# Optimization experiments

Measured on AMD Instinct MI355X. Metric: run time of the kernel, lower is better.

## Reference

```python
import jax, jax.numpy as jnp
import numpy as np

S, H, P, NL, PL = 128, 1024, 1024, 2, 32  # string_size, hidden, program_size, layers, program_length
T_IN, T_OUT = 64, 64


def _run_lstm(xs, h0, c0, layers):
    """Multi-layer LSTM over sequence xs [T, in]. PyTorch gate order i,f,g,o.
    h0, c0: [NL, H]. Returns (top-layer outputs [T, H], hT [NL,H], cT [NL,H])."""
    hs, cs = [], []
    for l, (Wih, Whh, bih, bhh) in enumerate(layers):
        b = bih + bhh
        def step(carry, x, Wih=Wih, Whh=Whh, b=b):
            h, c = carry
            g = Wih @ x + Whh @ h + b           # [4H]
            i, f, gg, o = jnp.split(g, 4)
            c = jax.nn.sigmoid(f) * c + jax.nn.sigmoid(i) * jnp.tanh(gg)
            h = jax.nn.sigmoid(o) * jnp.tanh(c)
            return (h, c), h
        (hT, cT), xs = jax.lax.scan(step, (h0[l], c0[l]), xs)
        hs.append(hT); cs.append(cT)
    return xs, jnp.stack(hs), jnp.stack(cs)


def setup_inputs() -> dict:
    key = jax.random.key(0)
    keys = iter(jax.random.split(key, 64))
    bound = 1.0 / np.sqrt(H)
    def u(shape):
        return jax.random.uniform(next(keys), shape, minval=-bound, maxval=bound, dtype=jnp.float32)
    d = {}
    for pre, in0 in (("in", S), ("out", S), ("pr", H)):
        for l in range(NL):
            isz = in0 if l == 0 else H
            d[f"{pre}_Wih{l}"] = u((4 * H, isz))
            d[f"{pre}_Whh{l}"] = u((4 * H, H))
            d[f"{pre}_bih{l}"] = u((4 * H,))
            d[f"{pre}_bhh{l}"] = u((4 * H,))
    d["lin_W"] = u((P, H))
    d["lin_b"] = u((P,))
    d["input_seq"] = jax.random.randint(next(keys), (T_IN,), 0, S)
    d["output_seq"] = jax.random.randint(next(keys), (T_OUT,), 0, S)
    return d


def reference(in_Wih0, in_Whh0, in_bih0, in_bhh0, in_Wih1, in_Whh1, in_bih1, in_bhh1,
              out_Wih0, out_Whh0, out_bih0, out_bhh0, out_Wih1, out_Whh1, out_bih1, out_bhh1,
              pr_Wih0, pr_Whh0, pr_bih0, pr_bhh0, pr_Wih1, pr_Whh1, pr_bih1, pr_bhh1,
              lin_W, lin_b, input_seq, output_seq):
    in_layers = [(in_Wih0, in_Whh0, in_bih0, in_bhh0), (in_Wih1, in_Whh1, in_bih1, in_bhh1)]
    out_layers = [(out_Wih0, out_Whh0, out_bih0, out_bhh0), (out_Wih1, out_Whh1, out_bih1, out_bhh1)]
    pr_layers = [(pr_Wih0, pr_Whh0, pr_bih0, pr_bhh0), (pr_Wih1, pr_Whh1, pr_bih1, pr_bhh1)]

    x_in = jax.nn.one_hot(input_seq, S, dtype=jnp.float32)    # [T_IN, S]
    x_out = jax.nn.one_hot(output_seq, S, dtype=jnp.float32)  # [T_OUT, S]

    h = jnp.zeros((NL, H), dtype=jnp.float32)
    c = jnp.zeros((NL, H), dtype=jnp.float32)
    _, h, c = _run_lstm(x_in, h, c, in_layers)
    _, h, c = _run_lstm(x_out, h, c, out_layers)

    # Faithful to source: previous_hidden is set once and never updated inside the loop,
    # so the program LSTM sees the SAME input vector at every decode step.
    prev_h = h[-1]                                            # [H]
    xs = jnp.broadcast_to(prev_h, (PL, H))
    ys, h, c = _run_lstm(xs, h, c, pr_layers)                 # [PL, H]
    return ys @ lin_W.T + lin_b                                # [PL, P]
```

## Files before the change

kernel.cpp:

```cpp
#include <hip/hip_runtime.h>
#include <hip/hip_fp16.h>
#include <cmath>

#define HDIM 1024
#define TPB 512
#define NWG 256
#define M4 4194304ull
#define WS_WOFF 327680ull
#define CVT_TOTAL 42991616ull
#define WS_NEEDED (WS_WOFF + CVT_TOTAL * 2ull)

typedef unsigned long long ulong64;
typedef unsigned int uint32;
typedef _Float16 h2f __attribute__((ext_vector_type(2)));

__device__ __forceinline__ ulong64 ld_g8(const ulong64* p) {
  return __hip_atomic_load(p, __ATOMIC_RELAXED, __HIP_MEMORY_SCOPE_AGENT);
}
__device__ __forceinline__ void st_gu(uint32* p, uint32 v) {
  __hip_atomic_store(p, v, __ATOMIC_RELAXED, __HIP_MEMORY_SCOPE_AGENT);
}
__device__ __forceinline__ void st_gi(int* p, int v) {
  __hip_atomic_store(p, v, __ATOMIC_RELAXED, __HIP_MEMORY_SCOPE_AGENT);
}

__device__ __forceinline__ float sigm(float x) { return 1.f / (1.f + __expf(-x)); }
__device__ __forceinline__ float tanh_f(float x) {
  float e = __expf(2.f * x);
  return 1.f - 2.f / (e + 1.f);
}

__device__ __forceinline__ float f4dot(float4 wf, float4 xf, float acc) {
  union { float4 f; h2f h[4]; } w, x;
  w.f = wf; x.f = xf;
#pragma unroll
  for (int i = 0; i < 4; ++i) {
#if __has_builtin(__builtin_amdgcn_fdot2)
    acc = __builtin_amdgcn_fdot2(w.h[i], x.h[i], acc, false);
#else
    acc = fmaf((float)w.h[i].x, (float)x.h[i].x, acc);
    acc = fmaf((float)w.h[i].y, (float)x.h[i].y, acc);
#endif
  }
  return acc;
}

__global__ void __launch_bounds__(TPB, 2) rf16_kernel(
    const float* __restrict__ in_Wih0, const float* __restrict__ in_bih0, const float* __restrict__ in_bhh0,
    const float* __restrict__ in_bih1, const float* __restrict__ in_bhh1,
    const float* __restrict__ out_Wih0, const float* __restrict__ out_bih0, const float* __restrict__ out_bhh0,
    const float* __restrict__ out_bih1, const float* __restrict__ out_bhh1,
    const float* __restrict__ pr_bih0, const float* __restrict__ pr_bhh0,
    const float* __restrict__ pr_bih1, const float* __restrict__ pr_bhh1,
    const float* __restrict__ lin_b,
    const int* __restrict__ in_seq, const int* __restrict__ out_seq,
    float* __restrict__ out, float* __restrict__ ws)
{
  const int tid = threadIdx.x, wg = blockIdx.x;
  const int wv = tid >> 6, lane = tid & 63;
  const int grp = lane >> 4, gl = lane & 15;
  const int cell = (wg << 2) + (wv & 3);
  const bool isL1 = wv < 4;
  const int rowi = (grp << 10) + cell;
  const bool chkWG = (wg < 8);

  const __half* wb = (const __half*)((const char*)ws + WS_WOFF);
  uint32* h0M = (uint32*)((char*)ws + 4096);
  uint32* h1M = (uint32*)((char*)ws + 20480);
  int* FL = (int*)((char*)ws + 36864);
  int* myFlag = FL + ((wg & 7) << 8);

  __shared__ __align__(16) ulong64 xaP[2][128], xbP[2][128];

  float c_reg = 0.f, pre0v = 0.f;
  float bA, bB, bC, lbias = 0.f;
  if (isL1) {
    bA = in_bih1[rowi] + in_bhh1[rowi];
    bB = out_bih1[rowi] + out_bhh1[rowi];
    bC = pr_bih1[rowi] + pr_bhh1[rowi];
  } else {
    bA = in_bih0[rowi] + in_bhh0[rowi];
    bB = out_bih0[rowi] + out_bhh0[rowi];
    bC = pr_bih0[rowi] + pr_bhh0[rowi];
    lbias = lin_b[cell];
  }

  int fail = 0;
  float4 wreg[16];
  float4 lw0, lw1;

  auto preload8 = [&](const __half* wrow, int base) {
    const float4* w4 = (const float4*)wrow;
#pragma unroll
    for (int j = 0; j < 8; ++j) wreg[base + j] = w4[j * 16 + gl];
  };
  auto dotx = [&](int base, const ulong64* xp, float acc) {
    const __half* x = (const __half*)xp;
#pragma unroll
    for (int j = 0; j < 8; ++j)
      acc = f4dot(wreg[base + j], *(const float4*)(x + (j * 16 + gl) * 8), acc);
    return acc;
  };
  auto red16 = [&](float v) {
#pragma unroll
    for (int o = 1; o < 16; o <<= 1) v += __shfl_xor(v, o, 64);
    return v;
  };
  auto wred64 = [&](float v) {
#pragma unroll
    for (int o = 1; o < 64; o <<= 1) v += __shfl_xor(v, o, 64);
    return v;
  };
  auto tags_ok = [&](const ulong64* d, int tag) {
    bool ok = true;
#pragma unroll
    for (int i = 0; i < 8; ++i)
      ok &= (((int)((d[i] >> 16) & 0xFFFF)) == tag) & (((int)(d[i] >> 48)) == tag);
    return ok;
  };
  auto pack_lds = [&](const ulong64* d, ulong64* dst) {
    uint32 q[8];
#pragma unroll
    for (int i = 0; i < 8; ++i)
      q[i] = (uint32)(d[i] & 0xFFFF) | ((uint32)((d[i] >> 32) & 0xFFFF) << 16);
    dst[4 * lane]     = (ulong64)q[0] | ((ulong64)q[1] << 32);
    dst[4 * lane + 1] = (ulong64)q[2] | ((ulong64)q[3] << 32);
    dst[4 * lane + 2] = (ulong64)q[4] | ((ulong64)q[5] << 32);
    dst[4 * lane + 3] = (ulong64)q[6] | ((ulong64)q[7] << 32);
  };
  auto fetch_pack = [&](const uint32* T, int stream, int tag, ulong64* dst) {
    if (fail) return;
    const int slot = tag & 3;
    if (chkWG) {
      const ulong64* sl = (const ulong64*)(T + (slot << 10)) + (wg << 6) + lane;
      int spins = 0;
      for (;;) {
        ulong64 w = ld_g8(sl);
        bool ok = (((int)((w >> 16) & 0xFFFF)) == tag) & (((int)(w >> 48)) == tag);
        if (__all(ok)) break;
        if (++spins > (1 << 20)) { fail = 1; break; }
      }
      if (!fail && lane < 8)
        st_gi(FL + (lane << 8) + (stream << 7) + (slot << 4) + wg, tag);
    }
    {
      const ulong64* fp = (const ulong64*)(myFlag + (stream << 7) + (slot << 4));
      int spins = 0;
      for (;;) {
        ulong64 f0 = ld_g8(fp), f1 = ld_g8(fp + 1);
        ulong64 f2 = ld_g8(fp + 2), f3 = ld_g8(fp + 3);
        bool ok = (((int)f0) == tag) & (((int)(f0 >> 32)) == tag) &
                  (((int)f1) == tag) & (((int)(f1 >> 32)) == tag) &
                  (((int)f2) == tag) & (((int)(f2 >> 32)) == tag) &
                  (((int)f3) == tag) & (((int)(f3 >> 32)) == tag);
        if (ok) break;
        if (++spins > (1 << 20)) { fail = 1; return; }
        __builtin_amdgcn_s_sleep(1);
      }
    }
    const ulong64* src = (const ulong64*)(T + (slot << 10)) + (lane << 3);
    ulong64 d[8];
    int spins = 0;
    for (;;) {
#pragma unroll
      for (int i = 0; i < 8; ++i) d[i] = ld_g8(src + i);
      if (__all(tags_ok(d, tag))) break;
      if (++spins > (1 << 16)) { fail = 1; return; }
    }
    pack_lds(d, dst);
  };
  auto zero_pack = [&](ulong64* dst) {
#pragma unroll
    for (int i = 0; i < 4; ++i) dst[4 * lane + i] = 0ull;
  };
  auto produce = [&](float v, uint32* T, int tag) {
    float gi = __shfl(v, 0, 64), gf = __shfl(v, 16, 64);
    float gc = __shfl(v, 32, 64), go = __shfl(v, 48, 64);
    float c2 = sigm(gf) * c_reg + sigm(gi) * tanh_f(gc);
    c_reg = c2;
    if (lane == 0) {
      uint32 w = ((uint32)tag << 16) | (uint32)__half_as_ushort(__float2half(sigm(go) * tanh_f(c2)));
      st_gu(T + ((tag & 3) << 10) + cell, w);
    }
  };

  if (!isL1) {
    int idx = in_seq[0];
    float v = bA + in_Wih0[(size_t)rowi * 128 + idx];
    produce(v, h0M, 1);
  }

  if (isL1) {
    preload8(wb + 0 * M4 + (size_t)rowi * 1024, 0);
    preload8(wb + 1 * M4 + (size_t)rowi * 1024, 8);
  } else {
    preload8(wb + 2 * M4 + (size_t)rowi * 1024, 0);
  }

#pragma unroll 1
  for (int s = 2; s <= 128; ++s) {
    if (s == 65 && !isL1) preload8(wb + 5 * M4 + (size_t)rowi * 1024, 0);
    if (s == 66 && isL1) {
      preload8(wb + 3 * M4 + (size_t)rowi * 1024, 0);
      preload8(wb + 4 * M4 + (size_t)rowi * 1024, 8);
    }
    float wcol = 0.f;
    if (!isL1) {
      int idx = (s < 65) ? in_seq[s - 1] : out_seq[s - 65];
      wcol = ((s < 65) ? in_Wih0 : out_Wih0)[(size_t)rowi * 128 + idx];
    }
    if (wv == 0) fetch_pack(h0M, 0, s - 1, xaP[s & 1]);
    if (wv == 1) {
      if (s == 2) zero_pack(xbP[0]);
      else fetch_pack(h1M, 1, s - 1, xbP[s & 1]);
    }
    __syncthreads();
    if (isL1) {
      float v = dotx(0, xaP[s & 1], 0.f);
      v = dotx(8, xbP[s & 1], v);
      v = red16(v) + ((s < 66) ? bA : bB);
      produce(v, h1M, s);
    } else {
      float v = red16(dotx(0, xaP[s & 1], 0.f)) + ((s < 65) ? bA : bB) + wcol;
      produce(v, h0M, s);
    }
  }

  if (wv == 0) fetch_pack(h0M, 0, 128, xaP[1]);
  if (wv == 1) fetch_pack(h1M, 1, 128, xbP[1]);
  __syncthreads();
  if (isL1) {
    float v = dotx(0, xaP[1], 0.f);
    v = dotx(8, xbP[1], v);
    v = red16(v) + bB;
    produce(v, h1M, 129);
  }

  if (!isL1) {
    preload8(wb + 9 * M4 + (size_t)rowi * 1024, 0);
    preload8(wb + 8 * M4 + (size_t)rowi * 1024, 8);
  }
  if (wv == 0) fetch_pack(h0M, 0, 128, xaP[0]);
  if (wv == 1) fetch_pack(h1M, 1, 129, xbP[0]);
  __syncthreads();
  if (!isL1) {
    pre0v = red16(dotx(0, xbP[0], 0.f)) + bC;
    float v = red16(dotx(8, xaP[0], 0.f)) + pre0v;
    produce(v, h0M, 130);
  }

  if (isL1) {
    preload8(wb + 6 * M4 + (size_t)rowi * 1024, 0);
    preload8(wb + 7 * M4 + (size_t)rowi * 1024, 8);
  } else {
#pragma unroll
    for (int j = 0; j < 8; ++j) wreg[j] = wreg[8 + j];
    const float4* lwp = (const float4*)(wb + 10 * M4 + (size_t)cell * 1024);
    lw0 = lwp[lane * 2]; lw1 = lwp[lane * 2 + 1];
  }

#pragma unroll 1
  for (int s = 131; s <= 162; ++s) {
    const int tb = (s == 131) ? 129 : s - 1;
    if (wv == 0) fetch_pack(h0M, 0, s - 1, xaP[s & 1]);
    if (wv == 1) fetch_pack(h1M, 1, tb, xbP[s & 1]);
    __syncthreads();
    if (isL1) {
      float v = dotx(0, xaP[s & 1], 0.f);
      v = dotx(8, xbP[s & 1], v);
      v = red16(v) + bC;
      produce(v, h1M, s);
    } else {
      if (s >= 132) {
        const __half* x = (const __half*)xbP[s & 1];
        float a = f4dot(lw0, *(const float4*)(x + lane * 16), 0.f);
        a = f4dot(lw1, *(const float4*)(x + lane * 16 + 8), a);
        float r = wred64(a) + lbias;
        if (lane == 0) out[(size_t)(s - 132) * 1024 + cell] = r;
      }
      if (s <= 161) {
        float v = red16(dotx(0, xaP[s & 1], 0.f)) + pre0v;
        produce(v, h0M, s);
      }
    }
  }

  if (wv == 1) fetch_pack(h1M, 1, 162, xbP[1]);
  __syncthreads();
  if (!isL1) {
    const __half* x = (const __half*)xbP[1];
    float a = f4dot(lw0, *(const float4*)(x + lane * 16), 0.f);
    a = f4dot(lw1, *(const float4*)(x + lane * 16 + 8), a);
    float r = wred64(a) + lbias;
    if (lane == 0) out[(size_t)31 * 1024 + cell] = r;
  }
}

struct CvtArgs { const float* s[11]; };

__global__ void __launch_bounds__(256) cvt_kernel(CvtArgs a, __half* dst) {
  size_t i = ((size_t)blockIdx.x * 256 + threadIdx.x) * 8;
  if (i >= CVT_TOTAL) return;
  const float* sp;
  if (i < 10 * M4) sp = a.s[i >> 22] + (i & (M4 - 1));
  else sp = a.s[10] + (i - 10 * M4);
  float4 f0 = ((const float4*)sp)[0];
  float4 f1 = ((const float4*)sp)[1];
  __half2 o[4];
  o[0] = __float22half2_rn(make_float2(f0.x, f0.y));
  o[1] = __float22half2_rn(make_float2(f0.z, f0.w));
  o[2] = __float22half2_rn(make_float2(f1.x, f1.y));
  o[3] = __float22half2_rn(make_float2(f1.z, f1.w));
  *((float4*)(dst + i)) = *(float4*)o;
}

extern "C" void kernel_launch(void* const* d_in, const int* in_sizes, int n_in,
                              void* d_out, int out_size, void* d_ws, size_t ws_size,
                              hipStream_t stream) {
  (void)in_sizes; (void)n_in; (void)out_size;
  if (ws_size < WS_NEEDED) return;
  (void)hipMemsetAsync(d_ws, 0, 45056, stream);
  const float* F[26];
  for (int i = 0; i < 26; ++i) F[i] = (const float*)d_in[i];
  const int* iseq = (const int*)d_in[26];
  const int* oseq = (const int*)d_in[27];

  CvtArgs ca;
  ca.s[0] = F[4];  ca.s[1] = F[5];  ca.s[2] = F[1];
  ca.s[3] = F[12]; ca.s[4] = F[13]; ca.s[5] = F[9];
  ca.s[6] = F[20]; ca.s[7] = F[21]; ca.s[8] = F[17];
  ca.s[9] = F[16]; ca.s[10] = F[24];
  __half* wdst = (__half*)((char*)d_ws + WS_WOFF);
  cvt_kernel<<<dim3((unsigned)(CVT_TOTAL / 8 / 256)), dim3(256), 0, stream>>>(ca, wdst);
  rf16_kernel<<<dim3(NWG), dim3(TPB), 0, stream>>>(
      F[0], F[2], F[3], F[6], F[7],
      F[8], F[10], F[11], F[14], F[15],
      F[18], F[19], F[22], F[23],
      F[25], iseq, oseq, (float*)d_out, (float*)d_ws);
}
```

Measured before the change: 654.6 us.

## Replace flag-based step barrier with replicated mirrored hidden-state buffers

Checker workgroups no longer publish per-slot flags that every workgroup polls before reading the shared hidden-state table. Instead they copy the validated tagged words into eight mirror copies, and each workgroup spins directly on its own mirror using the embedded tags. This removes one polling round-trip per timestep and spreads reads across replicas. The cost is eight times more store traffic per checker, a larger memset, and doubled LDS array declarations.

New measurement: 671.3 us. 2.5% more time.

```diff
diff --git a/kernel.cpp b/kernel.cpp
--- a/kernel.cpp
+++ b/kernel.cpp
@@ -17,10 +17,10 @@
 __device__ __forceinline__ ulong64 ld_g8(const ulong64* p) {
   return __hip_atomic_load(p, __ATOMIC_RELAXED, __HIP_MEMORY_SCOPE_AGENT);
 }
+__device__ __forceinline__ void st_g8(ulong64* p, ulong64 v) {
+  __hip_atomic_store(p, v, __ATOMIC_RELAXED, __HIP_MEMORY_SCOPE_AGENT);
+}
 __device__ __forceinline__ void st_gu(uint32* p, uint32 v) {
-  __hip_atomic_store(p, v, __ATOMIC_RELAXED, __HIP_MEMORY_SCOPE_AGENT);
-}
-__device__ __forceinline__ void st_gi(int* p, int v) {
   __hip_atomic_store(p, v, __ATOMIC_RELAXED, __HIP_MEMORY_SCOPE_AGENT);
 }
 
@@ -67,10 +67,11 @@
   const __half* wb = (const __half*)((const char*)ws + WS_WOFF);
   uint32* h0M = (uint32*)((char*)ws + 4096);
   uint32* h1M = (uint32*)((char*)ws + 20480);
-  int* FL = (int*)((char*)ws + 36864);
-  int* myFlag = FL + ((wg & 7) << 8);
-
-  __shared__ __align__(16) ulong64 xaP[2][128], xbP[2][128];
+  ulong64* h0Mir = (ulong64*)((char*)ws + 36864);
+  ulong64* h1Mir = (ulong64*)((char*)ws + 36864 + 131072);
+  const int myMir = (wg & 7) << 11;
+
+  __shared__ __align__(16) ulong64 xaP[2][256], xbP[2][256];
 
   float c_reg = 0.f, pre0v = 0.f;
   float bA, bB, bC, lbias = 0.f;
@@ -128,44 +129,35 @@
     dst[4 * lane + 2] = (ulong64)q[4] | ((ulong64)q[5] << 32);
     dst[4 * lane + 3] = (ulong64)q[6] | ((ulong64)q[7] << 32);
   };
-  auto fetch_pack = [&](const uint32* T, int stream, int tag, ulong64* dst) {
+  auto fetch_pack = [&](const uint32* T, ulong64* Mir, int tag, ulong64* dst) {
     if (fail) return;
     const int slot = tag & 3;
     if (chkWG) {
       const ulong64* sl = (const ulong64*)(T + (slot << 10)) + (wg << 6) + lane;
+      ulong64 w = 0;
       int spins = 0;
       for (;;) {
-        ulong64 w = ld_g8(sl);
+        w = ld_g8(sl);
         bool ok = (((int)((w >> 16) & 0xFFFF)) == tag) & (((int)(w >> 48)) == tag);
         if (__all(ok)) break;
         if (++spins > (1 << 20)) { fail = 1; break; }
       }
-      if (!fail && lane < 8)
-        st_gi(FL + (lane << 8) + (stream << 7) + (slot << 4) + wg, tag);
-    }
-    {
-      const ulong64* fp = (const ulong64*)(myFlag + (stream << 7) + (slot << 4));
-      int spins = 0;
-      for (;;) {
-        ulong64 f0 = ld_g8(fp), f1 = ld_g8(fp + 1);
-        ulong64 f2 = ld_g8(fp + 2), f3 = ld_g8(fp + 3);
-        bool ok = (((int)f0) == tag) & (((int)(f0 >> 32)) == tag) &
-                  (((int)f1) == tag) & (((int)(f1 >> 32)) == tag) &
-                  (((int)f2) == tag) & (((int)(f2 >> 32)) == tag) &
-                  (((int)f3) == tag) & (((int)(f3 >> 32)) == tag);
-        if (ok) break;
-        if (++spins > (1 << 20)) { fail = 1; return; }
-        __builtin_amdgcn_s_sleep(1);
+      if (!fail) {
+        const int widx = (slot << 9) + (wg << 6) + lane;
+#pragma unroll
+        for (int m = 0; m < 8; ++m)
+          st_g8(Mir + (m << 11) + widx, w);
       }
     }
-    const ulong64* src = (const ulong64*)(T + (slot << 10)) + (lane << 3);
+    const ulong64* src = Mir + myMir + (slot << 9) + (lane << 3);
     ulong64 d[8];
     int spins = 0;
     for (;;) {
 #pragma unroll
       for (int i = 0; i < 8; ++i) d[i] = ld_g8(src + i);
       if (__all(tags_ok(d, tag))) break;
-      if (++spins > (1 << 16)) { fail = 1; return; }
+      if (++spins > (1 << 20)) { fail = 1; return; }
+      __builtin_amdgcn_s_sleep(1);
     }
     pack_lds(d, dst);
   };
@@ -209,10 +201,10 @@
       int idx = (s < 65) ? in_seq[s - 1] : out_seq[s - 65];
       wcol = ((s < 65) ? in_Wih0 : out_Wih0)[(size_t)rowi * 128 + idx];
     }
-    if (wv == 0) fetch_pack(h0M, 0, s - 1, xaP[s & 1]);
+    if (wv == 0) fetch_pack(h0M, h0Mir, s - 1, xaP[s & 1]);
     if (wv == 1) {
       if (s == 2) zero_pack(xbP[0]);
-      else fetch_pack(h1M, 1, s - 1, xbP[s & 1]);
+      else fetch_pack(h1M, h1Mir, s - 1, xbP[s & 1]);
     }
     __syncthreads();
     if (isL1) {
@@ -226,8 +218,8 @@
     }
   }
 
-  if (wv == 0) fetch_pack(h0M, 0, 128, xaP[1]);
-  if (wv == 1) fetch_pack(h1M, 1, 128, xbP[1]);
+  if (wv == 0) fetch_pack(h0M, h0Mir, 128, xaP[1]);
+  if (wv == 1) fetch_pack(h1M, h1Mir, 128, xbP[1]);
   __syncthreads();
   if (isL1) {
     float v = dotx(0, xaP[1], 0.f);
@@ -240,8 +232,8 @@
     preload8(wb + 9 * M4 + (size_t)rowi * 1024, 0);
     preload8(wb + 8 * M4 + (size_t)rowi * 1024, 8);
   }
-  if (wv == 0) fetch_pack(h0M, 0, 128, xaP[0]);
-  if (wv == 1) fetch_pack(h1M, 1, 129, xbP[0]);
+  if (wv == 0) fetch_pack(h0M, h0Mir, 128, xaP[0]);
+  if (wv == 1) fetch_pack(h1M, h1Mir, 129, xbP[0]);
   __syncthreads();
   if (!isL1) {
     pre0v = red16(dotx(0, xbP[0], 0.f)) + bC;
@@ -262,8 +254,8 @@
 #pragma unroll 1
   for (int s = 131; s <= 162; ++s) {
     const int tb = (s == 131) ? 129 : s - 1;
-    if (wv == 0) fetch_pack(h0M, 0, s - 1, xaP[s & 1]);
-    if (wv == 1) fetch_pack(h1M, 1, tb, xbP[s & 1]);
+    if (wv == 0) fetch_pack(h0M, h0Mir, s - 1, xaP[s & 1]);
+    if (wv == 1) fetch_pack(h1M, h1Mir, tb, xbP[s & 1]);
     __syncthreads();
     if (isL1) {
       float v = dotx(0, xaP[s & 1], 0.f);
@@ -285,7 +277,7 @@
     }
   }
 
-  if (wv == 1) fetch_pack(h1M, 1, 162, xbP[1]);
+  if (wv == 1) fetch_pack(h1M, h1Mir, 162, xbP[1]);
   __syncthreads();
   if (!isL1) {
     const __half* x = (const __half*)xbP[1];
@@ -319,7 +311,7 @@
                               hipStream_t stream) {
   (void)in_sizes; (void)n_in; (void)out_size;
   if (ws_size < WS_NEEDED) return;
-  (void)hipMemsetAsync(d_ws, 0, 45056, stream);
+  (void)hipMemsetAsync(d_ws, 0, 299008, stream);
   const float* F[26];
   for (int i = 0; i < 26; ++i) F[i] = (const float*)d_in[i];
   const int* iseq = (const int*)d_in[26];
```

## Fuse fp32-to-fp16 weight conversion into the persistent LSTM kernel's register preloads

Applied to the files above, without the earlier changes.

Removes the separate conversion kernel that turned about 43M fp32 weights into fp16 in workspace. Each thread now reads its fp32 weight rows directly and converts them to half in registers during preload, for both the LSTM matrices and the final linear layer. This drops one full read-and-write pass over the weights and one kernel launch, and shrinks the workspace to the small flag/state area. In exchange, each preload inside the recurrence reads twice as many bytes, so the stalls at the sequence boundaries get longer. The shared-memory pack buffers are also doubled in size, and kernel arguments are now passed as a struct.

Measured after the change: 693.2 us. 5.9% more time.

```diff
diff --git a/kernel.cpp b/kernel.cpp
--- a/kernel.cpp
+++ b/kernel.cpp
@@ -5,10 +5,7 @@
 #define HDIM 1024
 #define TPB 512
 #define NWG 256
-#define M4 4194304ull
-#define WS_WOFF 327680ull
-#define CVT_TOTAL 42991616ull
-#define WS_NEEDED (WS_WOFF + CVT_TOTAL * 2ull)
+#define WS_NEEDED 45056ull
 
 typedef unsigned long long ulong64;
 typedef unsigned int uint32;
@@ -45,16 +42,22 @@
   return acc;
 }
 
-__global__ void __launch_bounds__(TPB, 2) rf16_kernel(
-    const float* __restrict__ in_Wih0, const float* __restrict__ in_bih0, const float* __restrict__ in_bhh0,
-    const float* __restrict__ in_bih1, const float* __restrict__ in_bhh1,
-    const float* __restrict__ out_Wih0, const float* __restrict__ out_bih0, const float* __restrict__ out_bhh0,
-    const float* __restrict__ out_bih1, const float* __restrict__ out_bhh1,
-    const float* __restrict__ pr_bih0, const float* __restrict__ pr_bhh0,
-    const float* __restrict__ pr_bih1, const float* __restrict__ pr_bhh1,
-    const float* __restrict__ lin_b,
-    const int* __restrict__ in_seq, const int* __restrict__ out_seq,
-    float* __restrict__ out, float* __restrict__ ws)
+__device__ __forceinline__ float4 cvt8(float4 a, float4 b) {
+  float4 r;
+  ((__half2*)&r)[0] = __float22half2_rn(make_float2(a.x, a.y));
+  ((__half2*)&r)[1] = __float22half2_rn(make_float2(a.z, a.w));
+  ((__half2*)&r)[2] = __float22half2_rn(make_float2(b.x, b.y));
+  ((__half2*)&r)[3] = __float22half2_rn(make_float2(b.z, b.w));
+  return r;
+}
+
+struct KArgs {
+  const float* W[26];
+  const int* iseq; const int* oseq;
+  float* out; float* ws;
+};
+
+__global__ void __launch_bounds__(TPB, 2) rf16_kernel(KArgs a)
 {
   const int tid = threadIdx.x, wg = blockIdx.x;
   const int wv = tid >> 6, lane = tid & 63;
@@ -64,35 +67,39 @@
   const int rowi = (grp << 10) + cell;
   const bool chkWG = (wg < 8);
 
-  const __half* wb = (const __half*)((const char*)ws + WS_WOFF);
+  float* ws = a.ws;
   uint32* h0M = (uint32*)((char*)ws + 4096);
   uint32* h1M = (uint32*)((char*)ws + 20480);
   int* FL = (int*)((char*)ws + 36864);
   int* myFlag = FL + ((wg & 7) << 8);
 
-  __shared__ __align__(16) ulong64 xaP[2][128], xbP[2][128];
+  __shared__ __align__(16) ulong64 xaP[2][256], xbP[2][256];
 
   float c_reg = 0.f, pre0v = 0.f;
   float bA, bB, bC, lbias = 0.f;
   if (isL1) {
-    bA = in_bih1[rowi] + in_bhh1[rowi];
-    bB = out_bih1[rowi] + out_bhh1[rowi];
-    bC = pr_bih1[rowi] + pr_bhh1[rowi];
+    bA = a.W[6][rowi] + a.W[7][rowi];
+    bB = a.W[14][rowi] + a.W[15][rowi];
+    bC = a.W[22][rowi] + a.W[23][rowi];
   } else {
-    bA = in_bih0[rowi] + in_bhh0[rowi];
-    bB = out_bih0[rowi] + out_bhh0[rowi];
-    bC = pr_bih0[rowi] + pr_bhh0[rowi];
-    lbias = lin_b[cell];
+    bA = a.W[2][rowi] + a.W[3][rowi];
+    bB = a.W[10][rowi] + a.W[11][rowi];
+    bC = a.W[18][rowi] + a.W[19][rowi];
+    lbias = a.W[25][cell];
   }
 
   int fail = 0;
   float4 wreg[16];
   float4 lw0, lw1;
 
-  auto preload8 = [&](const __half* wrow, int base) {
-    const float4* w4 = (const float4*)wrow;
-#pragma unroll
-    for (int j = 0; j < 8; ++j) wreg[base + j] = w4[j * 16 + gl];
+  auto preload8 = [&](const float* mat, int base) {
+    const float4* w4 = (const float4*)(mat + (size_t)rowi * 1024);
+#pragma unroll
+    for (int j = 0; j < 8; ++j) {
+      float4 p = w4[(j * 16 + gl) * 2];
+      float4 q = w4[(j * 16 + gl) * 2 + 1];
+      wreg[base + j] = cvt8(p, q);
+    }
   };
   auto dotx = [&](int base, const ulong64* xp, float acc) {
     const __half* x = (const __half*)xp;
@@ -185,29 +192,29 @@
   };
 
   if (!isL1) {
-    int idx = in_seq[0];
-    float v = bA + in_Wih0[(size_t)rowi * 128 + idx];
+    int idx = a.iseq[0];
+    float v = bA + a.W[0][(size_t)rowi * 128 + idx];
     produce(v, h0M, 1);
   }
 
   if (isL1) {
-    preload8(wb + 0 * M4 + (size_t)rowi * 1024, 0);
-    preload8(wb + 1 * M4 + (size_t)rowi * 1024, 8);
+    preload8(a.W[4], 0);
+    preload8(a.W[5], 8);
   } else {
-    preload8(wb + 2 * M4 + (size_t)rowi * 1024, 0);
+    preload8(a.W[1], 0);
   }
 
 #pragma unroll 1
   for (int s = 2; s <= 128; ++s) {
-    if (s == 65 && !isL1) preload8(wb + 5 * M4 + (size_t)rowi * 1024, 0);
+    if (s == 65 && !isL1) preload8(a.W[9], 0);
     if (s == 66 && isL1) {
-      preload8(wb + 3 * M4 + (size_t)rowi * 1024, 0);
-      preload8(wb + 4 * M4 + (size_t)rowi * 1024, 8);
+      preload8(a.W[12], 0);
+      preload8(a.W[13], 8);
     }
     float wcol = 0.f;
     if (!isL1) {
-      int idx = (s < 65) ? in_seq[s - 1] : out_seq[s - 65];
-      wcol = ((s < 65) ? in_Wih0 : out_Wih0)[(size_t)rowi * 128 + idx];
+      int idx = (s < 65) ? a.iseq[s - 1] : a.oseq[s - 65];
+      wcol = ((s < 65) ? a.W[0] : a.W[8])[(size_t)rowi * 128 + idx];
     }
     if (wv == 0) fetch_pack(h0M, 0, s - 1, xaP[s & 1]);
     if (wv == 1) {
@@ -237,8 +244,8 @@
   }
 
   if (!isL1) {
-    preload8(wb + 9 * M4 + (size_t)rowi * 1024, 0);
-    preload8(wb + 8 * M4 + (size_t)rowi * 1024, 8);
+    preload8(a.W[16], 0);
+    preload8(a.W[17], 8);
   }
   if (wv == 0) fetch_pack(h0M, 0, 128, xaP[0]);
   if (wv == 1) fetch_pack(h1M, 1, 129, xbP[0]);
@@ -250,13 +257,15 @@
   }
 
   if (isL1) {
-    preload8(wb + 6 * M4 + (size_t)rowi * 1024, 0);
-    preload8(wb + 7 * M4 + (size_t)rowi * 1024, 8);
+    preload8(a.W[20], 0);
+    preload8(a.W[21], 8);
   } else {
 #pragma unroll
     for (int j = 0; j < 8; ++j) wreg[j] = wreg[8 + j];
-    const float4* lwp = (const float4*)(wb + 10 * M4 + (size_t)cell * 1024);
-    lw0 = lwp[lane * 2]; lw1 = lwp[lane * 2 + 1];
+    const float4* lwp = (const float4*)(a.W[24] + (size_t)cell * 1024);
+    float4 a0 = lwp[lane * 4], a1 = lwp[lane * 4 + 1];
+    float4 a2 = lwp[lane * 4 + 2], a3 = lwp[lane * 4 + 3];
+    lw0 = cvt8(a0, a1); lw1 = cvt8(a2, a3);
   }
 
 #pragma unroll 1
@@ -273,10 +282,10 @@
     } else {
       if (s >= 132) {
         const __half* x = (const __half*)xbP[s & 1];
-        float a = f4dot(lw0, *(const float4*)(x + lane * 16), 0.f);
-        a = f4dot(lw1, *(const float4*)(x + lane * 16 + 8), a);
-        float r = wred64(a) + lbias;
-        if (lane == 0) out[(size_t)(s - 132) * 1024 + cell] = r;
+        float a0 = f4dot(lw0, *(const float4*)(x + lane * 16), 0.f);
+        a0 = f4dot(lw1, *(const float4*)(x + lane * 16 + 8), a0);
+        float r = wred64(a0) + lbias;
+        if (lane == 0) a.out[(size_t)(s - 132) * 1024 + cell] = r;
       }
       if (s <= 161) {
         float v = red16(dotx(0, xaP[s & 1], 0.f)) + pre0v;
@@ -289,29 +298,11 @@
   __syncthreads();
   if (!isL1) {
     const __half* x = (const __half*)xbP[1];
-    float a = f4dot(lw0, *(const float4*)(x + lane * 16), 0.f);
-    a = f4dot(lw1, *(const float4*)(x + lane * 16 + 8), a);
-    float r = wred64(a) + lbias;
-    if (lane == 0) out[(size_t)31 * 1024 + cell] = r;
-  }
-}
-
-struct CvtArgs { const float* s[11]; };
-
-__global__ void __launch_bounds__(256) cvt_kernel(CvtArgs a, __half* dst) {
-  size_t i = ((size_t)blockIdx.x * 256 + threadIdx.x) * 8;
-  if (i >= CVT_TOTAL) return;
-  const float* sp;
-  if (i < 10 * M4) sp = a.s[i >> 22] + (i & (M4 - 1));
-  else sp = a.s[10] + (i - 10 * M4);
-  float4 f0 = ((const float4*)sp)[0];
-  float4 f1 = ((const float4*)sp)[1];
-  __half2 o[4];
-  o[0] = __float22half2_rn(make_float2(f0.x, f0.y));
-  o[1] = __float22half2_rn(make_float2(f0.z, f0.w));
-  o[2] = __float22half2_rn(make_float2(f1.x, f1.y));
-  o[3] = __float22half2_rn(make_float2(f1.z, f1.w));
-  *((float4*)(dst + i)) = *(float4*)o;
+    float a0 = f4dot(lw0, *(const float4*)(x + lane * 16), 0.f);
+    a0 = f4dot(lw1, *(const float4*)(x + lane * 16 + 8), a0);
+    float r = wred64(a0) + lbias;
+    if (lane == 0) a.out[(size_t)31 * 1024 + cell] = r;
+  }
 }
 
 extern "C" void kernel_launch(void* const* d_in, const int* in_sizes, int n_in,
@@ -319,22 +310,12 @@
                               hipStream_t stream) {
   (void)in_sizes; (void)n_in; (void)out_size;
   if (ws_size < WS_NEEDED) return;
-  (void)hipMemsetAsync(d_ws, 0, 45056, stream);
-  const float* F[26];
-  for (int i = 0; i < 26; ++i) F[i] = (const float*)d_in[i];
-  const int* iseq = (const int*)d_in[26];
-  const int* oseq = (const int*)d_in[27];
-
-  CvtArgs ca;
-  ca.s[0] = F[4];  ca.s[1] = F[5];  ca.s[2] = F[1];
-  ca.s[3] = F[12]; ca.s[4] = F[13]; ca.s[5] = F[9];
-  ca.s[6] = F[20]; ca.s[7] = F[21]; ca.s[8] = F[17];
-  ca.s[9] = F[16]; ca.s[10] = F[24];
-  __half* wdst = (__half*)((char*)d_ws + WS_WOFF);
-  cvt_kernel<<<dim3((unsigned)(CVT_TOTAL / 8 / 256)), dim3(256), 0, stream>>>(ca, wdst);
-  rf16_kernel<<<dim3(NWG), dim3(TPB), 0, stream>>>(
-      F[0], F[2], F[3], F[6], F[7],
-      F[8], F[10], F[11], F[14], F[15],
-      F[18], F[19], F[22], F[23],
-      F[25], iseq, oseq, (float*)d_out, (float*)d_ws);
-}
+  (void)hipMemsetAsync(d_ws, 0, WS_NEEDED, stream);
+  KArgs a;
+  for (int i = 0; i < 26; ++i) a.W[i] = (const float*)d_in[i];
+  a.iseq = (const int*)d_in[26];
+  a.oseq = (const int*)d_in[27];
+  a.out = (float*)d_out;
+  a.ws = (float*)d_ws;
+  rf16_kernel<<<dim3(NWG), dim3(TPB), 0, stream>>>(a);
+}
```
